# Kernel tuning notes

Measured on AMD Instinct MI355X. Metric: run time of the kernel, lower is better.

Reference implementation:

```python
import jax, jax.numpy as jnp
import numpy as np

T, B, L, I, H = 1024, 1024, 10, 10, 10


def setup_inputs() -> dict:
    key = jax.random.key(0)
    ks = jax.random.split(key, 7)
    scale = 1.0 / np.sqrt(H)
    x = jax.random.normal(ks[0], (T, B, I), dtype=jnp.float32)
    hp = jax.random.normal(ks[1], (L, B, H), dtype=jnp.float32)
    cp = jax.random.normal(ks[2], (L, B, H), dtype=jnp.float32)
    # torch nn.LSTM params, uniform(-1/sqrt(H), 1/sqrt(H)); layer 0 input = I == H so all layers stack
    W_ih = jax.random.uniform(ks[3], (L, 4 * H, I), minval=-scale, maxval=scale, dtype=jnp.float32)
    W_hh = jax.random.uniform(ks[4], (L, 4 * H, H), minval=-scale, maxval=scale, dtype=jnp.float32)
    b_ih = jax.random.uniform(ks[5], (L, 4 * H), minval=-scale, maxval=scale, dtype=jnp.float32)
    b_hh = jax.random.uniform(ks[6], (L, 4 * H), minval=-scale, maxval=scale, dtype=jnp.float32)
    return {"x": x, "hp": hp, "cp": cp, "W_ih": W_ih, "W_hh": W_hh, "b_ih": b_ih, "b_hh": b_hh}


def _run_layer(inp, h0, c0, Wi, Wh, bi, bh):
    # precompute input projections for all timesteps: [T, B, 4H]
    xg = jnp.einsum('tbi,gi->tbg', inp, Wi) + bi + bh

    def step(carry, xg_t):
        h, c = carry
        g = xg_t + h @ Wh.T  # [B, 4H]; torch gate order: i, f, g, o
        i_g, f_g, g_g, o_g = jnp.split(g, 4, axis=-1)
        i_g = jax.nn.sigmoid(i_g)
        f_g = jax.nn.sigmoid(f_g)
        g_g = jnp.tanh(g_g)
        o_g = jax.nn.sigmoid(o_g)
        c = f_g * c + i_g * g_g
        h = o_g * jnp.tanh(c)
        return (h, c), h

    (hT, cT), ys = jax.lax.scan(step, (h0, c0), xg)
    return ys, hT, cT


def reference(x, hp, cp, W_ih, W_hh, b_ih, b_hh):
    out = x
    hns, cns = [], []
    for l in range(hp.shape[0]):  # fixed small layer stack
        out, hn, cn = _run_layer(out, hp[l], cp[l], W_ih[l], W_hh[l], b_ih[l], b_hh[l])
        hns.append(hn)
        cns.append(cn)
    return out, jnp.stack(hns), jnp.stack(cns)
```

## Files before the change

### kernel.cpp

```cpp
#include <hip/hip_runtime.h>

namespace {

constexpr int T = 1024;
constexpr int B = 1024;
constexpr int L = 10;
constexpr int H = 10;
constexpr int NTHREADS = 128;
constexpr int U = 4;
constexpr int NWIN = T / U;
constexpr int NINT = NWIN + L - 1;
constexpr int BH = B * H;
constexpr int WSLOT = 88;

using v2f = __attribute__((ext_vector_type(2))) float;

__device__ __forceinline__ v2f v2fma(v2f a, v2f b, v2f c) {
    return __builtin_elementwise_fma(a, b, c);
}

__device__ __forceinline__ float sigmoid_f(float x) {
    return __builtin_amdgcn_rcpf(1.0f + __expf(-x));
}
__device__ __forceinline__ float tanh_f(float x) {
    return 1.0f - 2.0f * __builtin_amdgcn_rcpf(1.0f + __expf(2.0f * x));
}

__global__
__attribute__((amdgpu_flat_work_group_size(NTHREADS, NTHREADS)))
__attribute__((amdgpu_waves_per_eu(2, 2)))
void lstm_pipeline(const float* __restrict__ x,
                   const float* __restrict__ hp,
                   const float* __restrict__ cp,
                   const float* __restrict__ Wih,
                   const float* __restrict__ Whh,
                   const float* __restrict__ bih,
                   const float* __restrict__ bhh,
                   float* __restrict__ out,
                   float* __restrict__ hn,
                   float* __restrict__ cn)
{
    __shared__ __align__(16) float wlds[L * H * WSLOT];
    __shared__ __align__(16) float buf[L + 1][2][U][12];
    __shared__ __align__(16) float hbuf[L][12];

    const int tid = threadIdx.x;
    const int wv = tid >> 6, ln = tid & 63;
    const bool active = (wv == 0) ? (ln < 60) : (ln < 40);
    const int lidx = (wv == 0) ? ln : 60 + ln;
    const int l = active ? lidx / 10 : L - 1;
    const int j = active ? lidx % 10 : H - 1;
    const int b = blockIdx.x;
    const int boff = b * H + j;

    if (active) {
        float* slot = &wlds[(l * H + j) * WSLOT];
        #pragma unroll
        for (int g = 0; g < 4; ++g) {
            const size_t row = (size_t)(l * 4 * H + g * H + j);
            const float* wr = Wih + row * H;
            const float* hr = Whh + row * H;
            #pragma unroll
            for (int i = 0; i < H; ++i) slot[g * H + i] = wr[i];
            #pragma unroll
            for (int i = 0; i < H; ++i) slot[40 + g * H + i] = hr[i];
            slot[80 + g] = bih[row] + bhh[row];
        }
    }
    __syncthreads();

    v2f wi2[4][5], wh2[4][5];
    float bias[4];
    {
        const float* slot = &wlds[(active ? l * H + j : 0) * WSLOT];
        #pragma unroll
        for (int g = 0; g < 4; ++g) {
            #pragma unroll
            for (int p = 0; p < 5; ++p) {
                v2f a; a[0] = slot[g * H + 2 * p];      a[1] = slot[g * H + 2 * p + 1];      wi2[g][p] = a;
                v2f d; d[0] = slot[40 + g * H + 2 * p]; d[1] = slot[40 + g * H + 2 * p + 1]; wh2[g][p] = d;
            }
            bias[g] = slot[80 + g];
        }
    }

    float h = 0.0f, c = 0.0f;
    float xcur[U], xnext[U];
    if (active) {
        h = hp[(l * B + b) * H + j];
        c = cp[(l * B + b) * H + j];
        hbuf[l][j] = h;
        if (l == 0) {
            #pragma unroll
            for (int u = 0; u < U; ++u) buf[0][1][u][j] = x[(size_t)u * BH + boff];
            #pragma unroll
            for (int u = 0; u < U; ++u) xcur[u] = x[(size_t)(U + u) * BH + boff];
        }
    }
    __syncthreads();

    for (int k = 0; k < NINT; ++k) {
        const int wp = k & 1, rp = wp ^ 1;
        if (active && l == 0 && (k + 2) < NWIN) {
            #pragma unroll
            for (int u = 0; u < U; ++u)
                xnext[u] = x[(size_t)((k + 2) * U + u) * BH + boff];
        }
        const unsigned w = (unsigned)(k - l);
        if (active && w < (unsigned)NWIN) {
            const int t0 = (int)w * U;
            #pragma unroll
            for (int u = 0; u < U; ++u) {
                float xin[12], hrow[12];
                {
                    const float4* xs = (const float4*)&buf[l][rp][u][0];
                    ((float4*)xin)[0] = xs[0]; ((float4*)xin)[1] = xs[1]; ((float4*)xin)[2] = xs[2];
                    const float4* hs = (const float4*)&hbuf[l][0];
                    ((float4*)hrow)[0] = hs[0]; ((float4*)hrow)[1] = hs[1]; ((float4*)hrow)[2] = hs[2];
                }
                v2f acc[4];
                #pragma unroll
                for (int g = 0; g < 4; ++g) { v2f a; a[0] = bias[g]; a[1] = 0.0f; acc[g] = a; }
                #pragma unroll
                for (int p = 0; p < 5; ++p) {
                    v2f xp; xp[0] = xin[2 * p]; xp[1] = xin[2 * p + 1];
                    #pragma unroll
                    for (int g = 0; g < 4; ++g) acc[g] = v2fma(wi2[g][p], xp, acc[g]);
                }
                #pragma unroll
                for (int p = 0; p < 5; ++p) {
                    v2f hh; hh[0] = hrow[2 * p]; hh[1] = hrow[2 * p + 1];
                    #pragma unroll
                    for (int g = 0; g < 4; ++g) acc[g] = v2fma(wh2[g][p], hh, acc[g]);
                }
                const float ig = sigmoid_f(acc[0][0] + acc[0][1]);
                const float fg = sigmoid_f(acc[1][0] + acc[1][1]);
                const float gg = tanh_f(acc[2][0] + acc[2][1]);
                const float og = sigmoid_f(acc[3][0] + acc[3][1]);
                c = fmaf(fg, c, ig * gg);
                h = og * tanh_f(c);

                hbuf[l][j] = h;
                if (l < L - 1) buf[l + 1][wp][u][j] = h;
                else out[(size_t)(t0 + u) * BH + boff] = h;
            }
        }
        if (active && l == 0 && (k + 1) < NWIN) {
            #pragma unroll
            for (int u = 0; u < U; ++u) buf[0][wp][u][j] = xcur[u];
            #pragma unroll
            for (int u = 0; u < U; ++u) xcur[u] = xnext[u];
        }
        __syncthreads();
    }

    if (active) {
        hn[(l * B + b) * H + j] = h;
        cn[(l * B + b) * H + j] = c;
    }
}

}

extern "C" void kernel_launch(void* const* d_in, const int* in_sizes, int n_in,
                              void* d_out, int out_size, void* d_ws, size_t ws_size,
                              hipStream_t stream) {
    (void)in_sizes; (void)n_in; (void)d_ws; (void)ws_size; (void)out_size;
    const float* x   = (const float*)d_in[0];
    const float* hp  = (const float*)d_in[1];
    const float* cp  = (const float*)d_in[2];
    const float* Wih = (const float*)d_in[3];
    const float* Whh = (const float*)d_in[4];
    const float* bih = (const float*)d_in[5];
    const float* bhh = (const float*)d_in[6];

    float* out = (float*)d_out;
    float* hn  = out + (size_t)T * B * H;
    float* cn  = hn + (size_t)L * B * H;

    lstm_pipeline<<<dim3(B), dim3(NTHREADS), 0, stream>>>(
        x, hp, cp, Wih, Whh, bih, bhh, out, hn, cn);
}
```

Baseline: 509.3 us.

## Drop per-lane activity predicates, pin weights in VGPRs, unroll ping-pong loop

Idle lanes are now mapped onto duplicate (layer, unit) slots, so every lane runs the same path. This removes the active-lane predicate from the hot loop, at the cost of redundant work and benign duplicate writes of identical values. Weights and biases are pinned in vector registers with empty asm constraints, and the waves-per-EU hint is relaxed to 1 to allow more registers. The time loop is unrolled by two so the double-buffer indices become compile-time constants. The last layer's output stores are batched after the four timesteps, and the weight slot stride shrinks so weights can be loaded as 2-float vectors.

```diff
diff --git a/kernel.cpp b/kernel.cpp
--- a/kernel.cpp
+++ b/kernel.cpp
@@ -11,13 +11,15 @@
 constexpr int NWIN = T / U;
 constexpr int NINT = NWIN + L - 1;
 constexpr int BH = B * H;
-constexpr int WSLOT = 88;
+constexpr int WSLOT = 84;
 
 using v2f = __attribute__((ext_vector_type(2))) float;
 
 __device__ __forceinline__ v2f v2fma(v2f a, v2f b, v2f c) {
     return __builtin_elementwise_fma(a, b, c);
 }
+__device__ __forceinline__ void pin2(v2f& v) { asm volatile("" : "+v"(v)); }
+__device__ __forceinline__ void pin1(float& v) { asm volatile("" : "+v"(v)); }
 
 __device__ __forceinline__ float sigmoid_f(float x) {
     return __builtin_amdgcn_rcpf(1.0f + __expf(-x));
@@ -28,7 +30,7 @@
 
 __global__
 __attribute__((amdgpu_flat_work_group_size(NTHREADS, NTHREADS)))
-__attribute__((amdgpu_waves_per_eu(2, 2)))
+__attribute__((amdgpu_waves_per_eu(1)))
 void lstm_pipeline(const float* __restrict__ x,
                    const float* __restrict__ hp,
                    const float* __restrict__ cp,
@@ -46,20 +48,21 @@
 
     const int tid = threadIdx.x;
     const int wv = tid >> 6, ln = tid & 63;
-    const bool active = (wv == 0) ? (ln < 60) : (ln < 40);
-    const int lidx = (wv == 0) ? ln : 60 + ln;
-    const int l = active ? lidx / 10 : L - 1;
-    const int j = active ? lidx % 10 : H - 1;
+    int lidx;
+    if (wv == 0) lidx = (ln < 60) ? ln : (ln - 10);
+    else         lidx = (ln < 40) ? (60 + ln) : (90 + (ln - 40) % 10);
+    const int l = lidx / 10;
+    const int j = lidx % 10;
     const int b = blockIdx.x;
     const int boff = b * H + j;
 
-    if (active) {
-        float* slot = &wlds[(l * H + j) * WSLOT];
+    {
+        float* slot = &wlds[lidx * WSLOT];
         #pragma unroll
         for (int g = 0; g < 4; ++g) {
-            const size_t row = (size_t)(l * 4 * H + g * H + j);
-            const float* wr = Wih + row * H;
-            const float* hr = Whh + row * H;
+            const int row = l * 4 * H + g * H + j;
+            const float* wr = Wih + (size_t)row * H;
+            const float* hr = Whh + (size_t)row * H;
             #pragma unroll
             for (int i = 0; i < H; ++i) slot[g * H + i] = wr[i];
             #pragma unroll
@@ -72,92 +75,114 @@
     v2f wi2[4][5], wh2[4][5];
     float bias[4];
     {
-        const float* slot = &wlds[(active ? l * H + j : 0) * WSLOT];
+        const float* slot = &wlds[lidx * WSLOT];
         #pragma unroll
         for (int g = 0; g < 4; ++g) {
             #pragma unroll
             for (int p = 0; p < 5; ++p) {
-                v2f a; a[0] = slot[g * H + 2 * p];      a[1] = slot[g * H + 2 * p + 1];      wi2[g][p] = a;
-                v2f d; d[0] = slot[40 + g * H + 2 * p]; d[1] = slot[40 + g * H + 2 * p + 1]; wh2[g][p] = d;
+                wi2[g][p] = *(const v2f*)&slot[g * H + 2 * p];
+                wh2[g][p] = *(const v2f*)&slot[40 + g * H + 2 * p];
             }
             bias[g] = slot[80 + g];
         }
     }
-
-    float h = 0.0f, c = 0.0f;
+    #pragma unroll
+    for (int g = 0; g < 4; ++g) {
+        #pragma unroll
+        for (int p = 0; p < 5; ++p) { pin2(wi2[g][p]); pin2(wh2[g][p]); }
+        pin1(bias[g]);
+    }
+
+    float h = hp[(l * B + b) * H + j];
+    float c = cp[(l * B + b) * H + j];
+    hbuf[l][j] = h;
+
     float xcur[U], xnext[U];
-    if (active) {
-        h = hp[(l * B + b) * H + j];
-        c = cp[(l * B + b) * H + j];
-        hbuf[l][j] = h;
-        if (l == 0) {
-            #pragma unroll
-            for (int u = 0; u < U; ++u) buf[0][1][u][j] = x[(size_t)u * BH + boff];
-            #pragma unroll
-            for (int u = 0; u < U; ++u) xcur[u] = x[(size_t)(U + u) * BH + boff];
-        }
+    if (lidx < 10) {
+        #pragma unroll
+        for (int u = 0; u < U; ++u) buf[0][1][u][j] = x[(size_t)u * BH + boff];
+        #pragma unroll
+        for (int u = 0; u < U; ++u) xcur[u] = x[(size_t)(U + u) * BH + boff];
     }
     __syncthreads();
 
-    for (int k = 0; k < NINT; ++k) {
-        const int wp = k & 1, rp = wp ^ 1;
-        if (active && l == 0 && (k + 2) < NWIN) {
+    auto interval = [&](int k, int wp, int rp) {
+        if (lidx < 10 && (k + 2) < NWIN) {
             #pragma unroll
             for (int u = 0; u < U; ++u)
                 xnext[u] = x[(size_t)((k + 2) * U + u) * BH + boff];
         }
         const unsigned w = (unsigned)(k - l);
-        if (active && w < (unsigned)NWIN) {
-            const int t0 = (int)w * U;
+        if (w < (unsigned)NWIN) {
+            float hv[U];
             #pragma unroll
             for (int u = 0; u < U; ++u) {
-                float xin[12], hrow[12];
+                float xin[10], hin[10];
                 {
-                    const float4* xs = (const float4*)&buf[l][rp][u][0];
-                    ((float4*)xin)[0] = xs[0]; ((float4*)xin)[1] = xs[1]; ((float4*)xin)[2] = xs[2];
-                    const float4* hs = (const float4*)&hbuf[l][0];
-                    ((float4*)hrow)[0] = hs[0]; ((float4*)hrow)[1] = hs[1]; ((float4*)hrow)[2] = hs[2];
+                    const float* xr = &buf[l][rp][u][0];
+                    *(float4*)&xin[0] = *(const float4*)(xr);
+                    *(float4*)&xin[4] = *(const float4*)(xr + 4);
+                    *(float2*)&xin[8] = *(const float2*)(xr + 8);
+                    const float* hr = &hbuf[l][0];
+                    *(float4*)&hin[0] = *(const float4*)(hr);
+                    *(float4*)&hin[4] = *(const float4*)(hr + 4);
+                    *(float2*)&hin[8] = *(const float2*)(hr + 8);
                 }
-                v2f acc[4];
-                #pragma unroll
-                for (int g = 0; g < 4; ++g) { v2f a; a[0] = bias[g]; a[1] = 0.0f; acc[g] = a; }
+                v2f a0, a1, a2, a3;
+                a0[0] = bias[0]; a0[1] = 0.0f;
+                a1[0] = bias[1]; a1[1] = 0.0f;
+                a2[0] = bias[2]; a2[1] = 0.0f;
+                a3[0] = bias[3]; a3[1] = 0.0f;
                 #pragma unroll
                 for (int p = 0; p < 5; ++p) {
                     v2f xp; xp[0] = xin[2 * p]; xp[1] = xin[2 * p + 1];
-                    #pragma unroll
-                    for (int g = 0; g < 4; ++g) acc[g] = v2fma(wi2[g][p], xp, acc[g]);
+                    a0 = v2fma(wi2[0][p], xp, a0);
+                    a1 = v2fma(wi2[1][p], xp, a1);
+                    a2 = v2fma(wi2[2][p], xp, a2);
+                    a3 = v2fma(wi2[3][p], xp, a3);
                 }
                 #pragma unroll
                 for (int p = 0; p < 5; ++p) {
-                    v2f hh; hh[0] = hrow[2 * p]; hh[1] = hrow[2 * p + 1];
-                    #pragma unroll
-                    for (int g = 0; g < 4; ++g) acc[g] = v2fma(wh2[g][p], hh, acc[g]);
+                    v2f hh; hh[0] = hin[2 * p]; hh[1] = hin[2 * p + 1];
+                    a0 = v2fma(wh2[0][p], hh, a0);
+                    a1 = v2fma(wh2[1][p], hh, a1);
+                    a2 = v2fma(wh2[2][p], hh, a2);
+                    a3 = v2fma(wh2[3][p], hh, a3);
                 }
-                const float ig = sigmoid_f(acc[0][0] + acc[0][1]);
-                const float fg = sigmoid_f(acc[1][0] + acc[1][1]);
-                const float gg = tanh_f(acc[2][0] + acc[2][1]);
-                const float og = sigmoid_f(acc[3][0] + acc[3][1]);
+                const float ig = sigmoid_f(a0[0] + a0[1]);
+                const float fg = sigmoid_f(a1[0] + a1[1]);
+                const float gg = tanh_f(a2[0] + a2[1]);
+                const float og = sigmoid_f(a3[0] + a3[1]);
                 c = fmaf(fg, c, ig * gg);
                 h = og * tanh_f(c);
 
                 hbuf[l][j] = h;
-                if (l < L - 1) buf[l + 1][wp][u][j] = h;
-                else out[(size_t)(t0 + u) * BH + boff] = h;
+                buf[l + 1][wp][u][j] = h;
+                hv[u] = h;
             }
-        }
-        if (active && l == 0 && (k + 1) < NWIN) {
+            if (l == L - 1) {
+                const int t0 = (int)w * U;
+                #pragma unroll
+                for (int u = 0; u < U; ++u)
+                    out[(size_t)(t0 + u) * BH + boff] = hv[u];
+            }
+        }
+        if (lidx < 10 && (k + 1) < NWIN) {
             #pragma unroll
             for (int u = 0; u < U; ++u) buf[0][wp][u][j] = xcur[u];
             #pragma unroll
             for (int u = 0; u < U; ++u) xcur[u] = xnext[u];
         }
         __syncthreads();
-    }
-
-    if (active) {
-        hn[(l * B + b) * H + j] = h;
-        cn[(l * B + b) * H + j] = c;
-    }
+    };
+
+    for (int kk = 0; kk < NINT + 1; kk += 2) {
+        interval(kk, 0, 1);
+        interval(kk + 1, 1, 0);
+    }
+
+    hn[(l * B + b) * H + j] = h;
+    cn[(l * B + b) * H + j] = c;
 }
 
 }
```

Result: no change. 499.8 us (-1.9%).
